# Kernel tuning notes

Hardware: AMD Instinct MI355X
Metric: run time of the kernel (lower is better)

The kernel has to match this reference:

```python
import jax, jax.numpy as jnp
import numpy as np

NUM_HEADS = 8


def _ln(x, w, b, eps=1e-5):
    mu = x.mean(-1, keepdims=True)
    var = ((x - mu) ** 2).mean(-1, keepdims=True)
    return (x - mu) * jax.lax.rsqrt(var + eps) * w + b


def _qkv(x, w, H, d):
    # x: (n, l, C) -> q,k,v each (n, H, l, d)
    n, l, _ = x.shape
    qkv = (x @ w.T).reshape(n, l, 3, H, d)
    qkv = jnp.transpose(qkv, (2, 0, 3, 1, 4))
    return qkv[0], qkv[1], qkv[2]


def _qkv_head(x, w, d):
    # x: (n, H, l, d) -> q,k,v each (n, H, l, d); linear acts on head_dim
    n, H, l, _ = x.shape
    qkv = (x @ w.T).reshape(n, H, l, 3, d)
    qkv = jnp.transpose(qkv, (3, 0, 1, 2, 4))
    return qkv[0], qkv[1], qkv[2]


def _attn(q, k, v, scale):
    s = jax.nn.softmax(jnp.einsum('nhqd,nhkd->nhqk', q, k) * scale, axis=-1)
    return jnp.einsum('nhqk,nhkd->nhqd', s, v)


def setup_inputs() -> dict:
    key = jax.random.key(0)
    ks = jax.random.split(key, 10)
    B, N, C = 16, 4096, 512
    l = 64
    H, d = NUM_HEADS, C // NUM_HEADS
    return {
        'x': jax.random.normal(ks[0], (B, N, C), jnp.float32),
        'n3_w': jnp.ones((C,), jnp.float32),
        'n3_b': jnp.zeros((C,), jnp.float32),
        'n4_w': jnp.ones((C,), jnp.float32),
        'n4_b': jnp.zeros((C,), jnp.float32),
        'ln1_w': jax.random.normal(ks[1], (3 * C, C), jnp.float32) * 0.02,
        'ln2_w': jax.random.normal(ks[2], (3 * C, C), jnp.float32) * 0.02,
        'ln3_w': jax.random.normal(ks[3], (3 * d, d), jnp.float32) * 0.02,
        'ln4_w': jax.random.normal(ks[4], (3 * d, d), jnp.float32) * 0.02,
        'pos1': jax.random.normal(ks[5], (1, l, C), jnp.float32),
        'pos2': jax.random.normal(ks[6], (1, l, C), jnp.float32),
        'pos3': jax.random.normal(ks[7], (1, H, l, d), jnp.float32),
        'pos4': jax.random.normal(ks[8], (1, H, l, d), jnp.float32),
    }


def reference(x, n3_w, n3_b, n4_w, n4_b, ln1_w, ln2_w, ln3_w, ln4_w,
              pos1, pos2, pos3, pos4):
    B, N, C = x.shape
    l = int(np.sqrt(N))
    H = NUM_HEADS
    d = C // H
    scale = d ** -0.5

    # window (row) branch
    x_w = _ln(x, n3_w, n3_b).reshape(B * l, l, C) + pos1
    q, k, v = _qkv(x_w, ln1_w, H, d)
    x_ww = _attn(q, k, v, scale) + pos3                     # (B*l, H, l, d)
    xw_q, xw_k, xw_v = _qkv_head(x_ww, ln3_w, d)

    # height (column) branch: transpose the l x l grid
    x_h = _ln(x, n4_w, n4_b).reshape(B, l, l, C)
    x_h = jnp.swapaxes(x_h, 1, 2).reshape(B * l, l, C) + pos2
    q, k, v = _qkv(x_h, ln2_w, H, d)
    x_hh = _attn(q, k, v, scale) + pos4
    xh_q, xh_k, xh_v = _qkv_head(x_hh, ln4_w, d)

    # cross-attention between the two axial branches
    o1 = _attn(xh_q, xw_k, xw_v, scale)                     # (B*l, H, l, d)
    o1 = jnp.swapaxes(o1, 1, 2).reshape(B, l, l, C)
    o1 = jnp.swapaxes(o1, 1, 2)
    o2 = _attn(xw_q, xh_k, xh_v, scale)
    o2 = jnp.swapaxes(o2, 1, 2).reshape(B, l, l, C)

    out = (o1 + o2).reshape(B, N, C) + x
    return out
```

## Files before the change

kernel.cpp:

```cpp
#include <hip/hip_runtime.h>
#include <hip/hip_bf16.h>

typedef unsigned short u16;
typedef __attribute__((ext_vector_type(8))) short bf16x8;
typedef __attribute__((ext_vector_type(4))) short bf16x4;
typedef __attribute__((ext_vector_type(4))) float floatx4;
typedef __attribute__((ext_vector_type(4))) unsigned short u16x4;

__device__ __forceinline__ float b2f(u16 u) {
  unsigned int i = ((unsigned int)u) << 16;
  return __builtin_bit_cast(float, i);
}
__device__ __forceinline__ u16 f2b(float f) {
  __hip_bfloat16 h = __float2bfloat16(f);
  return __builtin_bit_cast(u16, h);
}
#define MFMA16(a, b, c) __builtin_amdgcn_mfma_f32_16x16x32_bf16((a), (b), (c), 0, 0, 0)
#define LGKM0() __asm__ volatile("s_waitcnt lgkmcnt(0)" ::: "memory")
#define VM0() __asm__ volatile("s_waitcnt vmcnt(0)" ::: "memory")

#if __has_builtin(__builtin_amdgcn_mfma_f32_16x16x16bf16_1k)
#define HAVE_MFMA_K16 1
#define MFMA16K16(a, b, c) __builtin_amdgcn_mfma_f32_16x16x16bf16_1k((a), (b), (c), 0, 0, 0)
#else
#define HAVE_MFMA_K16 0
#endif

__device__ __forceinline__ void gload_lds16(const u16* g, u16* l) {
  __builtin_amdgcn_global_load_lds(
      (const __attribute__((address_space(1))) void*)g,
      (__attribute__((address_space(3))) void*)l, 16, 0, 0);
}

__global__ __launch_bounds__(256) void cvt_kernel(const float* __restrict__ a,
                                                  u16* __restrict__ o, int n4) {
  int i = blockIdx.x * 256 + threadIdx.x;
  if (i < n4) {
    float4 v = ((const float4*)a)[i];
    u16x4 r;
    r.x = f2b(v.x); r.y = f2b(v.y); r.z = f2b(v.z); r.w = f2b(v.w);
    ((u16x4*)o)[i] = r;
  }
}

__global__ __launch_bounds__(256) void ln_pos_kernel(
    const float* __restrict__ x, const float* __restrict__ n3w, const float* __restrict__ n3b,
    const float* __restrict__ n4w, const float* __restrict__ n4b,
    const float* __restrict__ pos1, const float* __restrict__ pos2,
    u16* __restrict__ yW, u16* __restrict__ yH) {
  int wv = threadIdx.x >> 6, lane = threadIdx.x & 63;
  int token = blockIdx.x * 4 + wv;
  int b = token >> 12, r = (token >> 6) & 63, c = token & 63;
  const float4* xr = (const float4*)(x + (size_t)token * 512) + lane * 2;
  float4 x0 = xr[0], x1 = xr[1];
  float v[8] = {x0.x, x0.y, x0.z, x0.w, x1.x, x1.y, x1.z, x1.w};
  float s = 0.f, ss = 0.f;
#pragma unroll
  for (int j = 0; j < 8; j++) { s += v[j]; ss += v[j] * v[j]; }
#pragma unroll
  for (int off = 1; off < 64; off <<= 1) { s += __shfl_xor(s, off); ss += __shfl_xor(ss, off); }
  float mu = s * (1.0f / 512.0f);
  float var = ss * (1.0f / 512.0f) - mu * mu;
  float rs = rsqrtf(var + 1e-5f);
  int ch0 = lane * 8;
  float w3[8], b3[8], w4[8], b4[8], p1[8], p2[8];
  *(float4*)&w3[0] = *(const float4*)(n3w + ch0); *(float4*)&w3[4] = *(const float4*)(n3w + ch0 + 4);
  *(float4*)&b3[0] = *(const float4*)(n3b + ch0); *(float4*)&b3[4] = *(const float4*)(n3b + ch0 + 4);
  *(float4*)&w4[0] = *(const float4*)(n4w + ch0); *(float4*)&w4[4] = *(const float4*)(n4w + ch0 + 4);
  *(float4*)&b4[0] = *(const float4*)(n4b + ch0); *(float4*)&b4[4] = *(const float4*)(n4b + ch0 + 4);
  const float* p1p = pos1 + (size_t)c * 512 + ch0;
  const float* p2p = pos2 + (size_t)r * 512 + ch0;
  *(float4*)&p1[0] = *(const float4*)p1p; *(float4*)&p1[4] = *(const float4*)(p1p + 4);
  *(float4*)&p2[0] = *(const float4*)p2p; *(float4*)&p2[4] = *(const float4*)(p2p + 4);
  bf16x8 ow, oh;
#pragma unroll
  for (int j = 0; j < 8; j++) {
    float xn = (v[j] - mu) * rs;
    ow[j] = (short)f2b(xn * w3[j] + b3[j] + p1[j]);
    oh[j] = (short)f2b(xn * w4[j] + b4[j] + p2[j]);
  }
  *(bf16x8*)(yW + (size_t)token * 512 + ch0) = ow;
  size_t hrow = (size_t)b * 4096 + (size_t)c * 64 + r;
  *(bf16x8*)(yH + hrow * 512 + ch0) = oh;
}

__global__ __launch_bounds__(256) void qkv_gemm_kernel(
    const u16* __restrict__ A0, const u16* __restrict__ A1,
    const u16* __restrict__ W0, const u16* __restrict__ W1,
    u16* __restrict__ Z0, u16* __restrict__ Z1) {
  const int K = 512, N = 1536;
  int br = blockIdx.z;
  const u16* A = br ? A1 : A0;
  const u16* W = br ? W1 : W0;
  u16* Z = br ? Z1 : Z0;
  int lin = blockIdx.y * 12 + blockIdx.x;
  int nl = (lin & 7) * 768 + (lin >> 3);
  int n0 = (nl % 12) * 128, m0 = (nl / 12) * 128;
  __shared__ u16 gpool[16384];
  int tid = threadIdx.x, lane = tid & 63, wave = tid >> 6;
  int wm = (wave >> 1) * 64, wn = (wave & 1) * 64;
  int ml = lane & 15, quad = lane >> 4;
  floatx4 acc[4][4];
#pragma unroll
  for (int mi = 0; mi < 4; mi++)
#pragma unroll
    for (int ni = 0; ni < 4; ni++) acc[mi][ni] = (floatx4){0.f, 0.f, 0.f, 0.f};

  int srow = (lane >> 2);
  int scol = (lane & 3) * 8;
  {
    u16 (*As)[32] = (u16(*)[32])gpool;
    u16 (*Bs)[32] = (u16(*)[32])(gpool + 4096);
#pragma unroll
    for (int i = 0; i < 2; i++) {
      int rbase = wave * 32 + i * 16;
      gload_lds16(A + (size_t)(m0 + rbase + srow) * K + scol, &As[rbase][0]);
      gload_lds16(W + (size_t)(n0 + rbase + srow) * K + scol, &Bs[rbase][0]);
    }
  }
  VM0();
  __syncthreads();
  for (int t = 0; t < 16; ++t) {
    u16* cb = gpool + (t & 1) * 8192;
    u16* nb = gpool + ((t & 1) ^ 1) * 8192;
    if (t < 15) {
      int kt = (t + 1) * 32;
      u16 (*As)[32] = (u16(*)[32])nb;
      u16 (*Bs)[32] = (u16(*)[32])(nb + 4096);
#pragma unroll
      for (int i = 0; i < 2; i++) {
        int rbase = wave * 32 + i * 16;
        gload_lds16(A + (size_t)(m0 + rbase + srow) * K + kt + scol, &As[rbase][0]);
        gload_lds16(W + (size_t)(n0 + rbase + srow) * K + kt + scol, &Bs[rbase][0]);
      }
    }
    u16 (*Asc)[32] = (u16(*)[32])cb;
    u16 (*Bsc)[32] = (u16(*)[32])(cb + 4096);
    bf16x8 a[4], bfr[4];
#pragma unroll
    for (int mi = 0; mi < 4; mi++) a[mi] = *(const bf16x8*)&Asc[wm + mi * 16 + ml][quad * 8];
#pragma unroll
    for (int ni = 0; ni < 4; ni++) bfr[ni] = *(const bf16x8*)&Bsc[wn + ni * 16 + ml][quad * 8];
#pragma unroll
    for (int mi = 0; mi < 4; mi++)
#pragma unroll
      for (int ni = 0; ni < 4; ni++) acc[mi][ni] = MFMA16(a[mi], bfr[ni], acc[mi][ni]);
    VM0();
    __syncthreads();
  }
  u16* wl = gpool + wave * 2048;
#pragma unroll
  for (int pair = 0; pair < 2; pair++) {
#pragma unroll
    for (int mh = 0; mh < 2; mh++) {
      int mi = pair * 2 + mh;
#pragma unroll
      for (int ni = 0; ni < 4; ni++)
#pragma unroll
        for (int r = 0; r < 4; r++)
          wl[(mh * 16 + quad * 4 + r) * 64 + ni * 16 + ml] = f2b(acc[mi][ni][r]);
    }
    LGKM0();
#pragma unroll
    for (int p = 0; p < 4; p++) {
      int lrow = p * 8 + (lane >> 3);
      int col8 = (lane & 7) * 8;
      bf16x8 vv = *(const bf16x8*)&wl[lrow * 64 + col8];
      int rg = m0 + wm + pair * 32 + lrow;
      *(bf16x8*)&Z[(size_t)rg * N + n0 + wn + col8] = vv;
    }
    LGKM0();
  }
}

__device__ __forceinline__ void attn_core(bf16x8 aq0, bf16x8 aq1,
                                          const u16 (*Ks)[72], const u16 (*Vt)[72],
                                          u16 (*Psw)[72], int lane, floatx4 o[4]) {
  int ml = lane & 15, quad = lane >> 4;
  floatx4 s[4];
#pragma unroll
  for (int nt = 0; nt < 4; nt++) {
    floatx4 z = (floatx4){0.f, 0.f, 0.f, 0.f};
    bf16x8 k0 = *(const bf16x8*)&Ks[nt * 16 + ml][quad * 8];
    bf16x8 k1 = *(const bf16x8*)&Ks[nt * 16 + ml][32 + quad * 8];
    z = MFMA16(k0, aq0, z);
    z = MFMA16(k1, aq1, z);
    s[nt] = z;
  }
  float m = -1e30f;
#pragma unroll
  for (int nt = 0; nt < 4; nt++)
#pragma unroll
    for (int r = 0; r < 4; r++) m = fmaxf(m, s[nt][r]);
  m = fmaxf(m, __shfl_xor(m, 16));
  m = fmaxf(m, __shfl_xor(m, 32));
  float mh = -m * 0.125f;
  float su = 0.f;
#pragma unroll
  for (int nt = 0; nt < 4; nt++)
#pragma unroll
    for (int r = 0; r < 4; r++) {
      float p = __expf(__builtin_fmaf(s[nt][r], 0.125f, mh));
      s[nt][r] = p; su += p;
    }
  su += __shfl_xor(su, 16);
  su += __shfl_xor(su, 32);
  float inv = 1.0f / su;
#if HAVE_MFMA_K16
  bf16x4 pa[4];
#pragma unroll
  for (int nt = 0; nt < 4; nt++)
#pragma unroll
    for (int r = 0; r < 4; r++) pa[nt][r] = (short)f2b(s[nt][r] * inv);
#pragma unroll
  for (int et = 0; et < 4; et++) {
    floatx4 z = (floatx4){0.f, 0.f, 0.f, 0.f};
#pragma unroll
    for (int nt = 0; nt < 4; nt++) {
      bf16x4 bv = *(const bf16x4*)&Vt[et * 16 + ml][nt * 16 + quad * 4];
      z = MFMA16K16(pa[nt], bv, z);
    }
    o[et] = z;
  }
#else
#pragma unroll
  for (int nt = 0; nt < 4; nt++)
#pragma unroll
    for (int r = 0; r < 4; r++)
      Psw[ml][nt * 16 + quad * 4 + r] = f2b(s[nt][r] * inv);
  LGKM0();
  bf16x8 ap0 = *(const bf16x8*)&Psw[ml][quad * 8];
  bf16x8 ap1 = *(const bf16x8*)&Psw[ml][32 + quad * 8];
#pragma unroll
  for (int et = 0; et < 4; et++) {
    floatx4 z = (floatx4){0.f, 0.f, 0.f, 0.f};
    bf16x8 b0 = *(const bf16x8*)&Vt[et * 16 + ml][quad * 8];
    bf16x8 b1 = *(const bf16x8*)&Vt[et * 16 + ml][32 + quad * 8];
    z = MFMA16(ap0, b0, z);
    z = MFMA16(ap1, b1, z);
    o[et] = z;
  }
#endif
}

__device__ __forceinline__ void head_qkv(const floatx4 o[4], const float* pp,
                                         const u16* lw, u16 (*Ks)[72], u16 (*Vt)[72],
                                         u16 (*Ps)[72], int wv, int lane,
                                         bf16x8& axq0, bf16x8& axq1) {
  int ml = lane & 15, quad = lane >> 4;
#pragma unroll
  for (int et = 0; et < 4; et++)
#pragma unroll
    for (int r = 0; r < 4; r++) {
      int qp = wv * 16 + quad * 4 + r, e = et * 16 + ml;
      Ps[quad * 4 + r][et * 16 + ml] = f2b(o[et][r] + pp[(size_t)qp * 64 + e]);
    }
  LGKM0();
  bf16x8 ax0 = *(const bf16x8*)&Ps[ml][quad * 8];
  bf16x8 ax1 = *(const bf16x8*)&Ps[ml][32 + quad * 8];
  LGKM0();
  __builtin_amdgcn_sched_barrier(0);
#pragma unroll
  for (int nj = 0; nj < 4; nj++) {
    int col = 64 + nj * 16 + ml;
    bf16x8 b0 = *(const bf16x8*)(lw + (size_t)col * 64 + quad * 8);
    bf16x8 b1 = *(const bf16x8*)(lw + (size_t)col * 64 + 32 + quad * 8);
    floatx4 z = (floatx4){0.f, 0.f, 0.f, 0.f};
    z = MFMA16(ax0, b0, z);
    z = MFMA16(ax1, b1, z);
#pragma unroll
    for (int r = 0; r < 4; r++)
      Ks[wv * 16 + quad * 4 + r][nj * 16 + ml] = f2b(z[r]);
  }
#pragma unroll
  for (int nj = 0; nj < 4; nj++) {
    int col = 128 + nj * 16 + ml;
    bf16x8 b0 = *(const bf16x8*)(lw + (size_t)col * 64 + quad * 8);
    bf16x8 b1 = *(const bf16x8*)(lw + (size_t)col * 64 + 32 + quad * 8);
    floatx4 z = (floatx4){0.f, 0.f, 0.f, 0.f};
    z = MFMA16(ax0, b0, z);
    z = MFMA16(ax1, b1, z);
#pragma unroll
    for (int r = 0; r < 4; r++)
      Vt[nj * 16 + ml][wv * 16 + quad * 4 + r] = f2b(z[r]);
  }
#pragma unroll
  for (int nj = 0; nj < 4; nj++) {
    int col = nj * 16 + ml;
    bf16x8 b0 = *(const bf16x8*)(lw + (size_t)col * 64 + quad * 8);
    bf16x8 b1 = *(const bf16x8*)(lw + (size_t)col * 64 + 32 + quad * 8);
    floatx4 z = (floatx4){0.f, 0.f, 0.f, 0.f};
    z = MFMA16(ax0, b0, z);
    z = MFMA16(ax1, b1, z);
#pragma unroll
    for (int r = 0; r < 4; r++)
      Ps[quad * 4 + r][nj * 16 + ml] = f2b(z[r]);
  }
  LGKM0();
  __builtin_amdgcn_sched_barrier(0);
  axq0 = *(const bf16x8*)&Ps[ml][quad * 8];
  axq1 = *(const bf16x8*)&Ps[ml][32 + quad * 8];
  LGKM0();
}

__global__ __launch_bounds__(256) void fused_attn_kernel(
    const u16* __restrict__ Zw, const u16* __restrict__ Zh,
    const u16* __restrict__ l3b, const u16* __restrict__ l4b,
    const float* __restrict__ pos3, const float* __restrict__ pos4,
    u16* __restrict__ o1b, u16* __restrict__ o2b) {
  int w = blockIdx.x, h = blockIdx.y;
  __shared__ u16 pool[23040];
  u16 (*KsW)[72] = (u16(*)[72])pool;
  u16 (*VtW)[72] = (u16(*)[72])(pool + 4608);
  u16 (*KsH)[72] = (u16(*)[72])(pool + 9216);
  u16 (*VtH)[72] = (u16(*)[72])(pool + 13824);
  int tid = threadIdx.x, lane = tid & 63, wv = tid >> 6;
  int ml = lane & 15, quad = lane >> 4;
  u16 (*Ps)[72] = (u16(*)[72])(pool + 18432 + wv * 1152);
  const u16* baseW = Zw + (size_t)w * 64 * 1536 + h * 64;
  const u16* baseH = Zh + (size_t)w * 64 * 1536 + h * 64;
  for (int i = tid; i < 512; i += 256) {
    int r = i >> 3, c = (i & 7) * 8;
    *(bf16x8*)&KsW[r][c] = *(const bf16x8*)(baseW + 512 + (size_t)r * 1536 + c);
    *(bf16x8*)&KsH[r][c] = *(const bf16x8*)(baseH + 512 + (size_t)r * 1536 + c);
  }
  for (int i = tid; i < 1024; i += 256) {
    int p = i >> 4, e0 = (i & 15) * 4;
    u16x4 vW = *(const u16x4*)(baseW + 1024 + (size_t)p * 1536 + e0);
    u16x4 vH = *(const u16x4*)(baseH + 1024 + (size_t)p * 1536 + e0);
    VtW[e0 + 0][p] = vW.x; VtW[e0 + 1][p] = vW.y; VtW[e0 + 2][p] = vW.z; VtW[e0 + 3][p] = vW.w;
    VtH[e0 + 0][p] = vH.x; VtH[e0 + 1][p] = vH.y; VtH[e0 + 2][p] = vH.z; VtH[e0 + 3][p] = vH.w;
  }
  const u16* qrW = baseW + (size_t)(wv * 16 + ml) * 1536 + quad * 8;
  const u16* qrH = baseH + (size_t)(wv * 16 + ml) * 1536 + quad * 8;
  bf16x8 aqW0 = *(const bf16x8*)qrW;
  bf16x8 aqW1 = *(const bf16x8*)(qrW + 32);
  bf16x8 aqH0 = *(const bf16x8*)qrH;
  bf16x8 aqH1 = *(const bf16x8*)(qrH + 32);
  __syncthreads();
  floatx4 oW[4], oH[4];
  attn_core(aqW0, aqW1, KsW, VtW, Ps, lane, oW);
  attn_core(aqH0, aqH1, KsH, VtH, Ps, lane, oH);
  __syncthreads();
  bf16x8 axqW0, axqW1, axqH0, axqH1;
  head_qkv(oW, pos3 + (size_t)h * 4096, l3b, KsW, VtW, Ps, wv, lane, axqW0, axqW1);
  __syncthreads();
  head_qkv(oH, pos4 + (size_t)h * 4096, l4b, KsH, VtH, Ps, wv, lane, axqH0, axqH1);
  __syncthreads();
  floatx4 c2[4], c1[4];
  attn_core(axqW0, axqW1, KsH, VtH, Ps, lane, c2);
  attn_core(axqH0, axqH1, KsW, VtW, Ps, lane, c1);
  __syncthreads();
  u16* Out1 = pool;
  u16* Out2 = pool + 4608;
#pragma unroll
  for (int et = 0; et < 4; et++)
#pragma unroll
    for (int r = 0; r < 4; r++) {
      int row = wv * 16 + quad * 4 + r;
      Out1[row * 64 + et * 16 + ml] = f2b(c1[et][r]);
      Out2[row * 64 + et * 16 + ml] = f2b(c2[et][r]);
    }
  __syncthreads();
  u16* o1p = o1b + (size_t)w * 32768 + h * 64;
  u16* o2p = o2b + (size_t)w * 32768 + h * 64;
#pragma unroll
  for (int j = 0; j < 2; j++) {
    int c = tid + j * 256;
    int pos = c >> 3, cc = (c & 7) * 8;
    *(bf16x8*)&o1p[(size_t)pos * 512 + cc] = *(const bf16x8*)&Out1[pos * 64 + cc];
    *(bf16x8*)&o2p[(size_t)pos * 512 + cc] = *(const bf16x8*)&Out2[pos * 64 + cc];
  }
}

__global__ __launch_bounds__(256) void final_add_kernel(
    const float* __restrict__ x, const u16* __restrict__ o1b,
    const u16* __restrict__ o2b, float* __restrict__ out) {
  int wv = threadIdx.x >> 6, lane = threadIdx.x & 63;
  int token = blockIdx.x * 4 + wv;
  int b = token >> 12, r = (token >> 6) & 63, c = token & 63;
  size_t i = (size_t)token * 512 + lane * 8;
  size_t i1 = ((size_t)b * 4096 + (size_t)c * 64 + r) * 512 + lane * 8;
  float vx[8];
  *(float4*)&vx[0] = *(const float4*)(x + i);
  *(float4*)&vx[4] = *(const float4*)(x + i + 4);
  bf16x8 v1 = *(const bf16x8*)(o1b + i1);
  bf16x8 v2 = *(const bf16x8*)(o2b + i);
  float vo[8];
#pragma unroll
  for (int j = 0; j < 8; j++)
    vo[j] = vx[j] + b2f((u16)v1[j]) + b2f((u16)v2[j]);
  *(float4*)(out + i) = *(float4*)&vo[0];
  *(float4*)(out + i + 4) = *(float4*)&vo[4];
}

extern "C" void kernel_launch(void* const* d_in, const int* in_sizes, int n_in,
                              void* d_out, int out_size, void* d_ws, size_t ws_size,
                              hipStream_t stream) {
  const float* x    = (const float*)d_in[0];
  const float* n3w  = (const float*)d_in[1];
  const float* n3b  = (const float*)d_in[2];
  const float* n4w  = (const float*)d_in[3];
  const float* n4b  = (const float*)d_in[4];
  const float* ln1  = (const float*)d_in[5];
  const float* ln2  = (const float*)d_in[6];
  const float* ln3  = (const float*)d_in[7];
  const float* ln4  = (const float*)d_in[8];
  const float* pos1 = (const float*)d_in[9];
  const float* pos2 = (const float*)d_in[10];
  const float* pos3 = (const float*)d_in[11];
  const float* pos4 = (const float*)d_in[12];

  char* ws = (char*)d_ws;
  u16* yW = (u16*)ws;
  u16* yH = (u16*)(ws + (size_t)67108864);
  u16* Zw = (u16*)(ws + (size_t)134217728);
  u16* Zh = (u16*)(ws + (size_t)335544320);
  u16* o1b = yW;
  u16* o2b = yH;
  float* out = (float*)d_out;

  u16* Wb1 = (u16*)d_out;
  u16* Wb2 = Wb1 + 786432;
  u16* l3b = Wb2 + 786432;
  u16* l4b = l3b + 12288;

  cvt_kernel<<<768, 256, 0, stream>>>(ln1, Wb1, 196608);
  cvt_kernel<<<768, 256, 0, stream>>>(ln2, Wb2, 196608);
  cvt_kernel<<<12, 256, 0, stream>>>(ln3, l3b, 3072);
  cvt_kernel<<<12, 256, 0, stream>>>(ln4, l4b, 3072);
  ln_pos_kernel<<<16384, 256, 0, stream>>>(x, n3w, n3b, n4w, n4b, pos1, pos2, yW, yH);
  qkv_gemm_kernel<<<dim3(12, 512, 2), 256, 0, stream>>>(yW, yH, Wb1, Wb2, Zw, Zh);
  fused_attn_kernel<<<dim3(1024, 8), 256, 0, stream>>>(Zw, Zh, l3b, l4b, pos3, pos4, o1b, o2b);
  final_add_kernel<<<16384, 256, 0, stream>>>(x, o1b, o2b, out);
}
```

Measured before the change: 879.1 us.

## Rework QKV GEMM into 256x256 tiles with swizzled LDS and staged prefetch

The QKV projection GEMM now uses 512-thread blocks computing 256x256 output tiles with K-steps of 64, double-buffered in 128KB of dynamic LDS. The LDS layout is XOR-swizzled to avoid bank conflicts, and global-to-LDS loads are split into quarters interleaved between MFMA phases, with partial vmcnt waits, raw barriers and s_setprio around the MFMA bursts. This targets lower global traffic per flop and better overlap of loads with matrix math. In exchange it runs one block per CU with high register pressure, and the schedule depends on a fragile barrier and waitcnt sequence.

```diff
diff --git a/kernel.cpp b/kernel.cpp
--- a/kernel.cpp
+++ b/kernel.cpp
@@ -18,6 +18,9 @@
 #define MFMA16(a, b, c) __builtin_amdgcn_mfma_f32_16x16x32_bf16((a), (b), (c), 0, 0, 0)
 #define LGKM0() __asm__ volatile("s_waitcnt lgkmcnt(0)" ::: "memory")
 #define VM0() __asm__ volatile("s_waitcnt vmcnt(0)" ::: "memory")
+#define BAR() do { __asm__ volatile("" ::: "memory"); \
+  __builtin_amdgcn_s_barrier(); \
+  __asm__ volatile("" ::: "memory"); } while (0)
 
 #if __has_builtin(__builtin_amdgcn_mfma_f32_16x16x16bf16_1k)
 #define HAVE_MFMA_K16 1
@@ -84,90 +87,129 @@
   *(bf16x8*)(yH + hrow * 512 + ch0) = oh;
 }
 
-__global__ __launch_bounds__(256) void qkv_gemm_kernel(
+__global__ __launch_bounds__(512, 1) void qkv_gemm_kernel(
     const u16* __restrict__ A0, const u16* __restrict__ A1,
     const u16* __restrict__ W0, const u16* __restrict__ W1,
     u16* __restrict__ Z0, u16* __restrict__ Z1) {
-  const int K = 512, N = 1536;
+  const int K = 512, N = 1536, NT = 8;
+  extern __shared__ u16 lds[];
   int br = blockIdx.z;
   const u16* A = br ? A1 : A0;
   const u16* W = br ? W1 : W0;
   u16* Z = br ? Z1 : Z0;
-  int lin = blockIdx.y * 12 + blockIdx.x;
-  int nl = (lin & 7) * 768 + (lin >> 3);
-  int n0 = (nl % 12) * 128, m0 = (nl / 12) * 128;
-  __shared__ u16 gpool[16384];
-  int tid = threadIdx.x, lane = tid & 63, wave = tid >> 6;
-  int wm = (wave >> 1) * 64, wn = (wave & 1) * 64;
+  int lin = blockIdx.y * 6 + blockIdx.x;
+  int nl = (lin & 7) * 192 + (lin >> 3);
+  int m0 = (nl / 6) * 256, n0 = (nl % 6) * 256;
+  int tid = threadIdx.x, lane = tid & 63, wv = tid >> 6;
+  int wm = wv >> 2, wn = wv & 3;
   int ml = lane & 15, quad = lane >> 4;
-  floatx4 acc[4][4];
-#pragma unroll
-  for (int mi = 0; mi < 4; mi++)
-#pragma unroll
-    for (int ni = 0; ni < 4; ni++) acc[mi][ni] = (floatx4){0.f, 0.f, 0.f, 0.f};
-
-  int srow = (lane >> 2);
-  int scol = (lane & 3) * 8;
-  {
-    u16 (*As)[32] = (u16(*)[32])gpool;
-    u16 (*Bs)[32] = (u16(*)[32])(gpool + 4096);
-#pragma unroll
-    for (int i = 0; i < 2; i++) {
-      int rbase = wave * 32 + i * 16;
-      gload_lds16(A + (size_t)(m0 + rbase + srow) * K + scol, &As[rbase][0]);
-      gload_lds16(W + (size_t)(n0 + rbase + srow) * K + scol, &Bs[rbase][0]);
-    }
-  }
-  VM0();
-  __syncthreads();
-  for (int t = 0; t < 16; ++t) {
-    u16* cb = gpool + (t & 1) * 8192;
-    u16* nb = gpool + ((t & 1) ^ 1) * 8192;
-    if (t < 15) {
-      int kt = (t + 1) * 32;
-      u16 (*As)[32] = (u16(*)[32])nb;
-      u16 (*Bs)[32] = (u16(*)[32])(nb + 4096);
-#pragma unroll
-      for (int i = 0; i < 2; i++) {
-        int rbase = wave * 32 + i * 16;
-        gload_lds16(A + (size_t)(m0 + rbase + srow) * K + kt + scol, &As[rbase][0]);
-        gload_lds16(W + (size_t)(n0 + rbase + srow) * K + kt + scol, &Bs[rbase][0]);
-      }
-    }
-    u16 (*Asc)[32] = (u16(*)[32])cb;
-    u16 (*Bsc)[32] = (u16(*)[32])(cb + 4096);
-    bf16x8 a[4], bfr[4];
-#pragma unroll
-    for (int mi = 0; mi < 4; mi++) a[mi] = *(const bf16x8*)&Asc[wm + mi * 16 + ml][quad * 8];
-#pragma unroll
-    for (int ni = 0; ni < 4; ni++) bfr[ni] = *(const bf16x8*)&Bsc[wn + ni * 16 + ml][quad * 8];
-#pragma unroll
-    for (int mi = 0; mi < 4; mi++)
-#pragma unroll
-      for (int ni = 0; ni < 4; ni++) acc[mi][ni] = MFMA16(a[mi], bfr[ni], acc[mi][ni]);
-    VM0();
-    __syncthreads();
-  }
-  u16* wl = gpool + wave * 2048;
-#pragma unroll
-  for (int pair = 0; pair < 2; pair++) {
+  int l8 = lane >> 3;
+  int scol = ((lane & 7) ^ l8) << 3;
+
+  floatx4 acc[8][4];
+#pragma unroll
+  for (int mi = 0; mi < 8; mi++)
+#pragma unroll
+    for (int n = 0; n < 4; n++) acc[mi][n] = (floatx4){0.f, 0.f, 0.f, 0.f};
+
+  auto stA = [&](int kt, int ab, int q) {
+    int row = (wv < 4) ? (q * 32 + wv * 8) : (128 + q * 32 + (wv - 4) * 8);
+    gload_lds16(A + (size_t)(m0 + row + l8) * K + kt + scol,
+                &lds[ab * 16384 + row * 64]);
+  };
+  auto stB = [&](int kt, int bb, int q) {
+    int row = q * 64 + wv * 8;
+    gload_lds16(W + (size_t)(n0 + row + l8) * K + kt + scol,
+                &lds[32768 + bb * 16384 + row * 64]);
+  };
+  auto rdA = [&](int ab, int row, int sl) {
+    return *(const bf16x8*)&lds[ab * 16384 + row * 64 + (((sl ^ (row & 7)) & 7) << 3)];
+  };
+  auto rdB = [&](int bb, int row, int sl) {
+    return *(const bf16x8*)&lds[32768 + bb * 16384 + row * 64 + (((sl ^ (row & 7)) & 7) << 3)];
+  };
+
+#pragma unroll
+  for (int q = 0; q < 4; q++) { stA(0, 0, q); stB(0, 0, q); }
+#pragma unroll
+  for (int q = 0; q < 3; q++) { stA(64, 1, q); stB(64, 1, q); }
+  __asm__ volatile("s_waitcnt vmcnt(6)" ::: "memory");
+  BAR();
+
+  for (int t = 0; t < NT; ++t) {
+    int b = t & 1;
+    bf16x8 bfr[4][2];
+    {
+      bf16x8 af[2][2];
+#pragma unroll
+      for (int n = 0; n < 4; n++)
+#pragma unroll
+        for (int kh = 0; kh < 2; kh++)
+          bfr[n][kh] = rdB(b, wn * 64 + n * 16 + ml, kh * 4 + quad);
+#pragma unroll
+      for (int mh = 0; mh < 2; mh++)
+#pragma unroll
+        for (int kh = 0; kh < 2; kh++)
+          af[mh][kh] = rdA(b, wm * 128 + mh * 16 + ml, kh * 4 + quad);
+      if (t + 1 < NT) { stA((t + 1) * 64, (t + 1) & 1, 3); stB((t + 1) * 64, (t + 1) & 1, 3); }
+      BAR();
+      __builtin_amdgcn_s_setprio(1);
+#pragma unroll
+      for (int mh = 0; mh < 2; mh++)
+#pragma unroll
+        for (int n = 0; n < 4; n++) {
+          acc[mh][n] = MFMA16(af[mh][0], bfr[n][0], acc[mh][n]);
+          acc[mh][n] = MFMA16(af[mh][1], bfr[n][1], acc[mh][n]);
+        }
+      __builtin_amdgcn_s_setprio(0);
+      BAR();
+    }
+#pragma unroll
+    for (int p = 1; p < 4; p++) {
+      bf16x8 af[2][2];
+#pragma unroll
+      for (int mh = 0; mh < 2; mh++)
+#pragma unroll
+        for (int kh = 0; kh < 2; kh++)
+          af[mh][kh] = rdA(b, wm * 128 + (p * 2 + mh) * 16 + ml, kh * 4 + quad);
+      if (t + 2 < NT) { stA((t + 2) * 64, b, p - 1); stB((t + 2) * 64, b, p - 1); }
+      BAR();
+      __builtin_amdgcn_s_setprio(1);
+#pragma unroll
+      for (int mh = 0; mh < 2; mh++)
+#pragma unroll
+        for (int n = 0; n < 4; n++) {
+          acc[p * 2 + mh][n] = MFMA16(af[mh][0], bfr[n][0], acc[p * 2 + mh][n]);
+          acc[p * 2 + mh][n] = MFMA16(af[mh][1], bfr[n][1], acc[p * 2 + mh][n]);
+        }
+      __builtin_amdgcn_s_setprio(0);
+      if (p < 3) BAR();
+    }
+    if (t + 2 < NT) { __asm__ volatile("s_waitcnt vmcnt(6)" ::: "memory"); }
+    else            { __asm__ volatile("s_waitcnt vmcnt(0)" ::: "memory"); }
+    BAR();
+  }
+
+  u16* wl = lds + wv * 2048;
+#pragma unroll
+  for (int mp = 0; mp < 4; mp++) {
 #pragma unroll
     for (int mh = 0; mh < 2; mh++) {
-      int mi = pair * 2 + mh;
-#pragma unroll
-      for (int ni = 0; ni < 4; ni++)
+      int mi = mp * 2 + mh;
+#pragma unroll
+      for (int n = 0; n < 4; n++)
 #pragma unroll
         for (int r = 0; r < 4; r++)
-          wl[(mh * 16 + quad * 4 + r) * 64 + ni * 16 + ml] = f2b(acc[mi][ni][r]);
+          wl[(mh * 16 + quad * 4 + r) * 64 + n * 16 + ml] = f2b(acc[mi][n][r]);
     }
     LGKM0();
 #pragma unroll
-    for (int p = 0; p < 4; p++) {
-      int lrow = p * 8 + (lane >> 3);
+    for (int p2 = 0; p2 < 4; p2++) {
+      int lrow = p2 * 8 + (lane >> 3);
       int col8 = (lane & 7) * 8;
       bf16x8 vv = *(const bf16x8*)&wl[lrow * 64 + col8];
-      int rg = m0 + wm + pair * 32 + lrow;
-      *(bf16x8*)&Z[(size_t)rg * N + n0 + wn + col8] = vv;
+      int rg = m0 + wm * 128 + mp * 32 + lrow;
+      *(bf16x8*)&Z[(size_t)rg * N + n0 + wn * 64 + col8] = vv;
     }
     LGKM0();
   }
@@ -425,12 +467,19 @@
   u16* l3b = Wb2 + 786432;
   u16* l4b = l3b + 12288;
 
+  static bool lds_attr_set = false;
+  if (!lds_attr_set) {
+    hipFuncSetAttribute((const void*)qkv_gemm_kernel,
+                        hipFuncAttributeMaxDynamicSharedMemorySize, 131072);
+    lds_attr_set = true;
+  }
+
   cvt_kernel<<<768, 256, 0, stream>>>(ln1, Wb1, 196608);
   cvt_kernel<<<768, 256, 0, stream>>>(ln2, Wb2, 196608);
   cvt_kernel<<<12, 256, 0, stream>>>(ln3, l3b, 3072);
   cvt_kernel<<<12, 256, 0, stream>>>(ln4, l4b, 3072);
   ln_pos_kernel<<<16384, 256, 0, stream>>>(x, n3w, n3b, n4w, n4b, pos1, pos2, yW, yH);
-  qkv_gemm_kernel<<<dim3(12, 512, 2), 256, 0, stream>>>(yW, yH, Wb1, Wb2, Zw, Zh);
+  qkv_gemm_kernel<<<dim3(6, 256, 2), 512, 131072, stream>>>(yW, yH, Wb1, Wb2, Zw, Zh);
   fused_attn_kernel<<<dim3(1024, 8), 256, 0, stream>>>(Zw, Zh, l3b, l4b, pos3, pos4, o1b, o2b);
   final_add_kernel<<<16384, 256, 0, stream>>>(x, o1b, o2b, out);
 }
```

Measured after the change: 823.5 us. -6.3%, faster.

## Fuse QKV projection GEMM into per-head attention kernel and merge weight conversions

Applied to the files above, without the earlier changes.

Removes the standalone QKV GEMM and its large Z intermediate buffers. Each attention block now computes its own head's Q, K and V directly from the layer-normed rows with MFMA, loading A fragments and weights straight from global memory. This avoids writing and re-reading a big intermediate. In exchange, A tiles are re-read once per head (8x), and weights come straight from global/L2 with no LDS tiling. The change also merges the four weight-conversion launches into one, remaps block IDs with XCD awareness, and drops a barrier between the two head_qkv calls.

```diff
diff --git a/kernel.cpp b/kernel.cpp
--- a/kernel.cpp
+++ b/kernel.cpp
@@ -17,7 +17,6 @@
 }
 #define MFMA16(a, b, c) __builtin_amdgcn_mfma_f32_16x16x32_bf16((a), (b), (c), 0, 0, 0)
 #define LGKM0() __asm__ volatile("s_waitcnt lgkmcnt(0)" ::: "memory")
-#define VM0() __asm__ volatile("s_waitcnt vmcnt(0)" ::: "memory")
 
 #if __has_builtin(__builtin_amdgcn_mfma_f32_16x16x16bf16_1k)
 #define HAVE_MFMA_K16 1
@@ -26,15 +25,17 @@
 #define HAVE_MFMA_K16 0
 #endif
 
-__device__ __forceinline__ void gload_lds16(const u16* g, u16* l) {
-  __builtin_amdgcn_global_load_lds(
-      (const __attribute__((address_space(1))) void*)g,
-      (__attribute__((address_space(3))) void*)l, 16, 0, 0);
-}
-
-__global__ __launch_bounds__(256) void cvt_kernel(const float* __restrict__ a,
-                                                  u16* __restrict__ o, int n4) {
-  int i = blockIdx.x * 256 + threadIdx.x;
+__global__ __launch_bounds__(256) void cvt_all_kernel(
+    const float* __restrict__ a1, u16* __restrict__ o1,
+    const float* __restrict__ a2, u16* __restrict__ o2,
+    const float* __restrict__ a3, u16* __restrict__ o3,
+    const float* __restrict__ a4, u16* __restrict__ o4) {
+  int b = blockIdx.x;
+  const float* a; u16* o; int i; int n4;
+  if (b < 768)       { a = a1; o = o1; i = b * 256 + threadIdx.x;          n4 = 196608; }
+  else if (b < 1536) { a = a2; o = o2; i = (b - 768) * 256 + threadIdx.x;  n4 = 196608; }
+  else if (b < 1548) { a = a3; o = o3; i = (b - 1536) * 256 + threadIdx.x; n4 = 3072; }
+  else               { a = a4; o = o4; i = (b - 1548) * 256 + threadIdx.x; n4 = 3072; }
   if (i < n4) {
     float4 v = ((const float4*)a)[i];
     u16x4 r;
@@ -84,95 +85,6 @@
   *(bf16x8*)(yH + hrow * 512 + ch0) = oh;
 }
 
-__global__ __launch_bounds__(256) void qkv_gemm_kernel(
-    const u16* __restrict__ A0, const u16* __restrict__ A1,
-    const u16* __restrict__ W0, const u16* __restrict__ W1,
-    u16* __restrict__ Z0, u16* __restrict__ Z1) {
-  const int K = 512, N = 1536;
-  int br = blockIdx.z;
-  const u16* A = br ? A1 : A0;
-  const u16* W = br ? W1 : W0;
-  u16* Z = br ? Z1 : Z0;
-  int lin = blockIdx.y * 12 + blockIdx.x;
-  int nl = (lin & 7) * 768 + (lin >> 3);
-  int n0 = (nl % 12) * 128, m0 = (nl / 12) * 128;
-  __shared__ u16 gpool[16384];
-  int tid = threadIdx.x, lane = tid & 63, wave = tid >> 6;
-  int wm = (wave >> 1) * 64, wn = (wave & 1) * 64;
-  int ml = lane & 15, quad = lane >> 4;
-  floatx4 acc[4][4];
-#pragma unroll
-  for (int mi = 0; mi < 4; mi++)
-#pragma unroll
-    for (int ni = 0; ni < 4; ni++) acc[mi][ni] = (floatx4){0.f, 0.f, 0.f, 0.f};
-
-  int srow = (lane >> 2);
-  int scol = (lane & 3) * 8;
-  {
-    u16 (*As)[32] = (u16(*)[32])gpool;
-    u16 (*Bs)[32] = (u16(*)[32])(gpool + 4096);
-#pragma unroll
-    for (int i = 0; i < 2; i++) {
-      int rbase = wave * 32 + i * 16;
-      gload_lds16(A + (size_t)(m0 + rbase + srow) * K + scol, &As[rbase][0]);
-      gload_lds16(W + (size_t)(n0 + rbase + srow) * K + scol, &Bs[rbase][0]);
-    }
-  }
-  VM0();
-  __syncthreads();
-  for (int t = 0; t < 16; ++t) {
-    u16* cb = gpool + (t & 1) * 8192;
-    u16* nb = gpool + ((t & 1) ^ 1) * 8192;
-    if (t < 15) {
-      int kt = (t + 1) * 32;
-      u16 (*As)[32] = (u16(*)[32])nb;
-      u16 (*Bs)[32] = (u16(*)[32])(nb + 4096);
-#pragma unroll
-      for (int i = 0; i < 2; i++) {
-        int rbase = wave * 32 + i * 16;
-        gload_lds16(A + (size_t)(m0 + rbase + srow) * K + kt + scol, &As[rbase][0]);
-        gload_lds16(W + (size_t)(n0 + rbase + srow) * K + kt + scol, &Bs[rbase][0]);
-      }
-    }
-    u16 (*Asc)[32] = (u16(*)[32])cb;
-    u16 (*Bsc)[32] = (u16(*)[32])(cb + 4096);
-    bf16x8 a[4], bfr[4];
-#pragma unroll
-    for (int mi = 0; mi < 4; mi++) a[mi] = *(const bf16x8*)&Asc[wm + mi * 16 + ml][quad * 8];
-#pragma unroll
-    for (int ni = 0; ni < 4; ni++) bfr[ni] = *(const bf16x8*)&Bsc[wn + ni * 16 + ml][quad * 8];
-#pragma unroll
-    for (int mi = 0; mi < 4; mi++)
-#pragma unroll
-      for (int ni = 0; ni < 4; ni++) acc[mi][ni] = MFMA16(a[mi], bfr[ni], acc[mi][ni]);
-    VM0();
-    __syncthreads();
-  }
-  u16* wl = gpool + wave * 2048;
-#pragma unroll
-  for (int pair = 0; pair < 2; pair++) {
-#pragma unroll
-    for (int mh = 0; mh < 2; mh++) {
-      int mi = pair * 2 + mh;
-#pragma unroll
-      for (int ni = 0; ni < 4; ni++)
-#pragma unroll
-        for (int r = 0; r < 4; r++)
-          wl[(mh * 16 + quad * 4 + r) * 64 + ni * 16 + ml] = f2b(acc[mi][ni][r]);
-    }
-    LGKM0();
-#pragma unroll
-    for (int p = 0; p < 4; p++) {
-      int lrow = p * 8 + (lane >> 3);
-      int col8 = (lane & 7) * 8;
-      bf16x8 vv = *(const bf16x8*)&wl[lrow * 64 + col8];
-      int rg = m0 + wm + pair * 32 + lrow;
-      *(bf16x8*)&Z[(size_t)rg * N + n0 + wn + col8] = vv;
-    }
-    LGKM0();
-  }
-}
-
 __device__ __forceinline__ void attn_core(bf16x8 aq0, bf16x8 aq1,
                                           const u16 (*Ks)[72], const u16 (*Vt)[72],
                                           u16 (*Psw)[72], int lane, floatx4 o[4]) {
@@ -243,6 +155,80 @@
 #endif
 }
 
+__device__ __forceinline__ void gemm_qkv512(
+    const u16* __restrict__ yrow,
+    const u16* __restrict__ Wq,
+    u16 (*Ks)[72], u16 (*Vt)[72], u16 (*Ps)[72],
+    int wv, int lane, bf16x8& aq0, bf16x8& aq1) {
+  int ml = lane & 15, quad = lane >> 4;
+  const u16* ya = yrow + (size_t)ml * 512 + quad * 8;
+  bf16x8 a[16];
+#pragma unroll
+  for (int kk = 0; kk < 16; kk++) a[kk] = *(const bf16x8*)(ya + kk * 32);
+  {
+    floatx4 acc[4];
+#pragma unroll
+    for (int ct = 0; ct < 4; ct++) acc[ct] = (floatx4){0.f, 0.f, 0.f, 0.f};
+#pragma unroll
+    for (int ct = 0; ct < 4; ct++) {
+      const u16* wr = Wq + (size_t)(ct * 16 + ml) * 512 + quad * 8;
+#pragma unroll
+      for (int kk = 0; kk < 16; kk++) {
+        bf16x8 b = *(const bf16x8*)(wr + kk * 32);
+        acc[ct] = MFMA16(a[kk], b, acc[ct]);
+      }
+    }
+#pragma unroll
+    for (int ct = 0; ct < 4; ct++)
+#pragma unroll
+      for (int r = 0; r < 4; r++)
+        Ps[quad * 4 + r][ct * 16 + ml] = f2b(acc[ct][r]);
+    LGKM0();
+    aq0 = *(const bf16x8*)&Ps[ml][quad * 8];
+    aq1 = *(const bf16x8*)&Ps[ml][32 + quad * 8];
+    LGKM0();
+    __builtin_amdgcn_sched_barrier(0);
+  }
+  {
+    floatx4 acc[4];
+#pragma unroll
+    for (int ct = 0; ct < 4; ct++) acc[ct] = (floatx4){0.f, 0.f, 0.f, 0.f};
+#pragma unroll
+    for (int ct = 0; ct < 4; ct++) {
+      const u16* wr = Wq + 262144 + (size_t)(ct * 16 + ml) * 512 + quad * 8;
+#pragma unroll
+      for (int kk = 0; kk < 16; kk++) {
+        bf16x8 b = *(const bf16x8*)(wr + kk * 32);
+        acc[ct] = MFMA16(a[kk], b, acc[ct]);
+      }
+    }
+#pragma unroll
+    for (int ct = 0; ct < 4; ct++)
+#pragma unroll
+      for (int r = 0; r < 4; r++)
+        Ks[wv * 16 + quad * 4 + r][ct * 16 + ml] = f2b(acc[ct][r]);
+  }
+  {
+    floatx4 acc[4];
+#pragma unroll
+    for (int ct = 0; ct < 4; ct++) acc[ct] = (floatx4){0.f, 0.f, 0.f, 0.f};
+#pragma unroll
+    for (int ct = 0; ct < 4; ct++) {
+      const u16* wr = Wq + 524288 + (size_t)(ct * 16 + ml) * 512 + quad * 8;
+#pragma unroll
+      for (int kk = 0; kk < 16; kk++) {
+        bf16x8 b = *(const bf16x8*)(wr + kk * 32);
+        acc[ct] = MFMA16(a[kk], b, acc[ct]);
+      }
+    }
+#pragma unroll
+    for (int ct = 0; ct < 4; ct++)
+#pragma unroll
+      for (int r = 0; r < 4; r++)
+        Vt[ct * 16 + ml][wv * 16 + quad * 4 + r] = f2b(acc[ct][r]);
+  }
+}
+
 __device__ __forceinline__ void head_qkv(const floatx4 o[4], const float* pp,
                                          const u16* lw, u16 (*Ks)[72], u16 (*Vt)[72],
                                          u16 (*Ps)[72], int wv, int lane,
@@ -303,12 +289,15 @@
   LGKM0();
 }
 
-__global__ __launch_bounds__(256) void fused_attn_kernel(
-    const u16* __restrict__ Zw, const u16* __restrict__ Zh,
+__global__ __launch_bounds__(256) void fused_qkv_attn_kernel(
+    const u16* __restrict__ yW, const u16* __restrict__ yH,
+    const u16* __restrict__ Wb1, const u16* __restrict__ Wb2,
     const u16* __restrict__ l3b, const u16* __restrict__ l4b,
     const float* __restrict__ pos3, const float* __restrict__ pos4,
     u16* __restrict__ o1b, u16* __restrict__ o2b) {
-  int w = blockIdx.x, h = blockIdx.y;
+  int id = blockIdx.x;
+  int xcd = id & 7, slot = id >> 3;
+  int h = slot & 7, w = (slot >> 3) * 8 + xcd;
   __shared__ u16 pool[23040];
   u16 (*KsW)[72] = (u16(*)[72])pool;
   u16 (*VtW)[72] = (u16(*)[72])(pool + 4608);
@@ -317,26 +306,11 @@
   int tid = threadIdx.x, lane = tid & 63, wv = tid >> 6;
   int ml = lane & 15, quad = lane >> 4;
   u16 (*Ps)[72] = (u16(*)[72])(pool + 18432 + wv * 1152);
-  const u16* baseW = Zw + (size_t)w * 64 * 1536 + h * 64;
-  const u16* baseH = Zh + (size_t)w * 64 * 1536 + h * 64;
-  for (int i = tid; i < 512; i += 256) {
-    int r = i >> 3, c = (i & 7) * 8;
-    *(bf16x8*)&KsW[r][c] = *(const bf16x8*)(baseW + 512 + (size_t)r * 1536 + c);
-    *(bf16x8*)&KsH[r][c] = *(const bf16x8*)(baseH + 512 + (size_t)r * 1536 + c);
-  }
-  for (int i = tid; i < 1024; i += 256) {
-    int p = i >> 4, e0 = (i & 15) * 4;
-    u16x4 vW = *(const u16x4*)(baseW + 1024 + (size_t)p * 1536 + e0);
-    u16x4 vH = *(const u16x4*)(baseH + 1024 + (size_t)p * 1536 + e0);
-    VtW[e0 + 0][p] = vW.x; VtW[e0 + 1][p] = vW.y; VtW[e0 + 2][p] = vW.z; VtW[e0 + 3][p] = vW.w;
-    VtH[e0 + 0][p] = vH.x; VtH[e0 + 1][p] = vH.y; VtH[e0 + 2][p] = vH.z; VtH[e0 + 3][p] = vH.w;
-  }
-  const u16* qrW = baseW + (size_t)(wv * 16 + ml) * 1536 + quad * 8;
-  const u16* qrH = baseH + (size_t)(wv * 16 + ml) * 1536 + quad * 8;
-  bf16x8 aqW0 = *(const bf16x8*)qrW;
-  bf16x8 aqW1 = *(const bf16x8*)(qrW + 32);
-  bf16x8 aqH0 = *(const bf16x8*)qrH;
-  bf16x8 aqH1 = *(const bf16x8*)(qrH + 32);
+  bf16x8 aqW0, aqW1, aqH0, aqH1;
+  gemm_qkv512(yW + ((size_t)w * 64 + wv * 16) * 512, Wb1 + (size_t)h * 32768,
+              KsW, VtW, Ps, wv, lane, aqW0, aqW1);
+  gemm_qkv512(yH + ((size_t)w * 64 + wv * 16) * 512, Wb2 + (size_t)h * 32768,
+              KsH, VtH, Ps, wv, lane, aqH0, aqH1);
   __syncthreads();
   floatx4 oW[4], oH[4];
   attn_core(aqW0, aqW1, KsW, VtW, Ps, lane, oW);
@@ -344,7 +318,6 @@
   __syncthreads();
   bf16x8 axqW0, axqW1, axqH0, axqH1;
   head_qkv(oW, pos3 + (size_t)h * 4096, l3b, KsW, VtW, Ps, wv, lane, axqW0, axqW1);
-  __syncthreads();
   head_qkv(oH, pos4 + (size_t)h * 4096, l4b, KsH, VtH, Ps, wv, lane, axqH0, axqH1);
   __syncthreads();
   floatx4 c2[4], c1[4];
@@ -412,12 +385,10 @@
   const float* pos4 = (const float*)d_in[12];
 
   char* ws = (char*)d_ws;
-  u16* yW = (u16*)ws;
-  u16* yH = (u16*)(ws + (size_t)67108864);
-  u16* Zw = (u16*)(ws + (size_t)134217728);
-  u16* Zh = (u16*)(ws + (size_t)335544320);
-  u16* o1b = yW;
-  u16* o2b = yH;
+  u16* yW  = (u16*)ws;
+  u16* yH  = (u16*)(ws + (size_t)67108864);
+  u16* o1b = (u16*)(ws + (size_t)134217728);
+  u16* o2b = (u16*)(ws + (size_t)201326592);
   float* out = (float*)d_out;
 
   u16* Wb1 = (u16*)d_out;
@@ -425,12 +396,9 @@
   u16* l3b = Wb2 + 786432;
   u16* l4b = l3b + 12288;
 
-  cvt_kernel<<<768, 256, 0, stream>>>(ln1, Wb1, 196608);
-  cvt_kernel<<<768, 256, 0, stream>>>(ln2, Wb2, 196608);
-  cvt_kernel<<<12, 256, 0, stream>>>(ln3, l3b, 3072);
-  cvt_kernel<<<12, 256, 0, stream>>>(ln4, l4b, 3072);
+  cvt_all_kernel<<<1560, 256, 0, stream>>>(ln1, Wb1, ln2, Wb2, ln3, l3b, ln4, l4b);
   ln_pos_kernel<<<16384, 256, 0, stream>>>(x, n3w, n3b, n4w, n4b, pos1, pos2, yW, yH);
-  qkv_gemm_kernel<<<dim3(12, 512, 2), 256, 0, stream>>>(yW, yH, Wb1, Wb2, Zw, Zh);
-  fused_attn_kernel<<<dim3(1024, 8), 256, 0, stream>>>(Zw, Zh, l3b, l4b, pos3, pos4, o1b, o2b);
+  fused_qkv_attn_kernel<<<8192, 256, 0, stream>>>(yW, yH, Wb1, Wb2, l3b, l4b,
+                                                  pos3, pos4, o1b, o2b);
   final_add_kernel<<<16384, 256, 0, stream>>>(x, o1b, o2b, out);
 }
```

New measurement: 2.037 ms. +131.8%, slower.
